# Kernel tuning notes

Measured on AMD Instinct MI355X. Metric: run time of the kernel, lower is better.

Reference implementation:

```python
import jax, jax.numpy as jnp
import numpy as np

N, E, D, H, T, R, K = 40000, 320000, 128, 4, 3, 5, 3
DK = D // H
SQRT_DK = float(np.sqrt(DK))

def _glorot(key, shape):
    lim = float(np.sqrt(6.0 / (shape[-2] + shape[-1])))
    return jax.random.uniform(key, shape, jnp.float32, -lim, lim)

def setup_inputs():
    ks = jax.random.split(jax.random.key(0), 16)
    return {
        "meta_xs": jax.random.normal(ks[0], (N, D), jnp.float32),
        "node_type": jax.random.randint(ks[1], (N,), 0, T),
        "edge_index": jax.random.randint(ks[2], (2, E), 0, N),
        "edge_type": jax.random.randint(ks[3], (E,), 0, R),
        "edge_time": jax.random.randint(ks[4], (E,), 0, 100),
        "q_w": _glorot(ks[5], (T, D, D)), "q_b": jnp.zeros((T, D), jnp.float32),
        "k_w": _glorot(ks[6], (T, D, D)), "k_b": jnp.zeros((T, D), jnp.float32),
        "v_w": _glorot(ks[7], (T, D, D)), "v_b": jnp.zeros((T, D), jnp.float32),
        "a_w": _glorot(ks[8], (T, D, D)), "a_b": jnp.zeros((T, D), jnp.float32),
        "rel_pri": jnp.ones((R, H), jnp.float32),
        "rel_att": _glorot(ks[9], (R, H, DK, DK)),
        "rel_msg": _glorot(ks[10], (R, H, DK, DK)),
        "WMk": _glorot(ks[11], (K, D, D)),
        "Wak": _glorot(ks[12], (K, D, D)),
        "Wq": _glorot(ks[13], (D, D)), "bq": jnp.zeros((D,), jnp.float32),
        "Wkl": _glorot(ks[14], (D, D)), "bkl": jnp.zeros((D,), jnp.float32),
        "skip": jnp.ones((T,), jnp.float32),
        "ln_g": jnp.ones((T, D), jnp.float32),
        "ln_b": jnp.zeros((T, D), jnp.float32),
    }

def _forward(meta_xs, q_w, q_b, k_w, k_b, v_w, v_b, a_w, a_b, rel_pri, rel_att,
             rel_msg, WMk, Wak, Wq, bq, Wkl, bkl, skip, ln_g, ln_b,
             node_type, edge_index, edge_type):
    src, tgt = edge_index[0], edge_index[1]
    ar = jnp.arange(N)

    def typed(x, W, b):  # per-node-type linear: equivalent to the type-masked loops
        all_t = jnp.einsum('ni,tio->tno', x, W)        # [T, N, D]
        return all_t[node_type, ar] + b[node_type]      # [N, D]

    qn = typed(meta_xs, q_w, q_b).reshape(N, H, DK)
    kn = typed(meta_xs, k_w, k_b).reshape(N, H, DK)
    vn = typed(meta_xs, v_w, v_b).reshape(N, H, DK)
    qe, ke, ve = qn[tgt], kn[src], vn[src]              # [E, H, DK]

    # relation-specific bmm, honoring per-relation dispatch without [E,H,DK,DK] gather
    kp = jnp.zeros_like(ke)
    vp = jnp.zeros_like(ve)
    for r in range(R):
        sel = (edge_type == r)[:, None, None]
        kp = jnp.where(sel, jnp.einsum('ehd,hdm->ehm', ke, rel_att[r]), kp)
        vp = jnp.where(sel, jnp.einsum('ehd,hdm->ehm', ve, rel_msg[r]), vp)

    logits = (qe * kp).sum(-1) * rel_pri[edge_type] / SQRT_DK   # [E, H]
    # segment softmax over incoming edges per target node (torch_geometric softmax)
    mx = jax.ops.segment_max(logits, tgt, num_segments=N)
    ex = jnp.exp(logits - mx[tgt])
    att = ex / (jax.ops.segment_sum(ex, tgt, num_segments=N)[tgt] + 1e-16)

    # power-moment expanded, attention-weighted messages: [K, E, D]
    msgs = jnp.stack([((vp ** (kk + 1)) * att[:, :, None]).reshape(E, D) for kk in range(K)])

    # faithful to original aggregate(): messages indexed by target node id (not edge id)
    agg = jnp.stack([jax.ops.segment_sum(msgs[kk][tgt], tgt, num_segments=N) for kk in range(K)])
    # faithful: only the last moment gets the signed K-th root (loop re-clones each iter)
    root = jnp.sign(agg[K - 1]) * (jnp.abs(agg[K - 1]) + 1e-18) ** (1.0 / K)
    aggm = agg.at[K - 1].set(root)
    aggm = jnp.einsum('knd,kde->kne', aggm, WMk)        # [K, N, D]

    qlin = meta_xs @ Wq + bq
    res = jnp.zeros((N, D), meta_xs.dtype)
    for kk in range(K):
        front = qlin @ Wak[kk]                          # [N, D]
        tail = aggm[kk] @ Wkl + bkl                     # [N, D]
        t = jax.nn.sigmoid((front * tail).sum(-1))      # [N]
        res = res + t[:, None] * aggm[kk]

    # update(): gelu -> per-type linear -> learned skip -> per-type LayerNorm
    h = jax.nn.gelu(res, approximate=False)
    trans = typed(h, a_w, a_b)
    alpha = jax.nn.sigmoid(skip)[node_type][:, None]
    y = trans * alpha + meta_xs * (1.0 - alpha)
    mu = y.mean(-1, keepdims=True)
    var = ((y - mu) ** 2).mean(-1, keepdims=True)
    y = (y - mu) / jnp.sqrt(var + 1e-5) * ln_g[node_type] + ln_b[node_type]
    return y

def reference(meta_xs, node_type, edge_index, edge_type, edge_time,
              q_w, q_b, k_w, k_b, v_w, v_b, a_w, a_b, rel_pri, rel_att, rel_msg,
              WMk, Wak, Wq, bq, Wkl, bkl, skip, ln_g, ln_b):
    return _forward(meta_xs, q_w, q_b, k_w, k_b, v_w, v_b, a_w, a_b, rel_pri,
                    rel_att, rel_msg, WMk, Wak, Wq, bq, Wkl, bkl, skip, ln_g, ln_b,
                    node_type, edge_index, edge_type)
```

## Files before the change

kernel.cpp:

```cpp
#include <hip/hip_runtime.h>

#define N_ 40000
#define E_ 320000
#define D_ 128
#define H_ 4
#define T_ 3
#define R_ 5

typedef unsigned short u16;

__device__ __forceinline__ float bf2f(u16 h){ return __uint_as_float(((unsigned)h)<<16); }
__device__ __forceinline__ u16 f2bf(float f){
  unsigned u = __float_as_uint(f);
  u += 0x7fffu + ((u>>16)&1u);
  return (u16)(u>>16);
}
__device__ __forceinline__ unsigned fmono(float f){
  unsigned u = __float_as_uint(f);
  return (u>>31) ? ~u : (u | 0x80000000u);
}
__device__ __forceinline__ float monof(unsigned u){
  return (u>>31) ? __uint_as_float(u & 0x7fffffffu) : __uint_as_float(~u);
}
__device__ __forceinline__ float ldx(const void* p, long i, int f32){
  return f32 ? ((const float*)p)[i] : bf2f(((const u16*)p)[i]);
}
__device__ __forceinline__ float wredsum(float v){
  #pragma unroll
  for (int m=32;m;m>>=1) v += __shfl_xor(v, m, 64);
  return v;
}

#define W_QW 0
#define W_KW 49152
#define W_VW 98304
#define W_AW 147456
#define W_QB 196608
#define W_KB 196992
#define W_VB 197376
#define W_AB 197760
#define W_PRI 198144
#define W_RATT 198164
#define W_RMSG 218644
#define W_WMK 239124
#define W_WAK 288276
#define W_WQ 337428
#define W_BQ 353812
#define W_WKL 353940
#define W_BKL 370324
#define W_SKIP 370452
#define W_LNG 370455
#define W_LNB 370839
#define W_TOT 371223

#define OFF_FLAGS 0ul
#define OFF_WCF   512ul
#define OFF_NT32  1485824ul
#define OFF_EI32  1646080ul
#define OFF_ET32  4206592ul
#define OFF_PERM  5486592ul
#define OFF_PCNT  5647360ul
#define OFF_TVAL  5647872ul
#define OFF_NPERM 5737984ul
#define OFF_LOG   6288384ul
#define OFF_QN    12848640ul
#define OFF_KN    33328640ul
#define OFF_VN    53808640ul
#define OFF_QLIN  74288640ul
#define OFF_QTR   94768640ul

__global__ __launch_bounds__(256) void detect_kernel(
    const u16* __restrict__ xs, const int* __restrict__ nt, int* __restrict__ flags)
{
  __shared__ int sBig, sZero, sNz;
  int tid = threadIdx.x;
  if (tid==0){ sBig=0; sZero=0; sNz=0; }
  __syncthreads();
  int big=0, zc=0;
  for (int i=tid; i<1024; i+=256) {
    u16 v = xs[2*i];
    int e = (v>>7)&0xFF;
    big += (e >= 200);
    zc  += (v == 0);
  }
  int nz=0;
  for (int i=tid; i<1024; i+=256) nz += (nt[2*i+1] != 0);
  atomicAdd(&sBig, big); atomicAdd(&sZero, zc); atomicAdd(&sNz, nz);
  __syncthreads();
  if (tid==0) {
    flags[0] = (sBig > 64) || (sZero > 900);
    flags[1] = (sNz == 0);
  }
}

struct FPtrs { const void* p[20]; };
__global__ __launch_bounds__(256) void convf_kernel(
    const int* __restrict__ flags, FPtrs ptrs, float* __restrict__ wcf)
{
  const int start[21] = {0,49152,98304,147456,196608,196992,197376,197760,198144,
    198164,218644,239124,288276,337428,353812,353940,370324,370452,370455,370839,371223};
  int i = blockIdx.x*256 + threadIdx.x;
  if (i >= W_TOT) return;
  int arr = 0;
  #pragma unroll
  for (int a=1; a<20; ++a) arr += (i >= start[a]);
  int local = i - start[arr];
  wcf[i] = ldx(ptrs.p[arr], local, flags[0]);
}

__global__ __launch_bounds__(256) void idxconv_kernel(
    const int* __restrict__ flags,
    const int* __restrict__ nt, const int* __restrict__ ei, const int* __restrict__ et,
    int* __restrict__ nt32, int* __restrict__ ei32, int* __restrict__ et32)
{
  int i = blockIdx.x*256 + threadIdx.x;
  if (i >= 1000000) return;
  int w = flags[1] ? 2 : 1;
  if (i < 40000)        nt32[i] = nt[(long)i*w];
  else if (i < 680000)  { int j=i-40000;  ei32[j] = ei[(long)j*w]; }
  else                  { int j=i-680000; et32[j] = et[(long)j*w]; }
}

__global__ __launch_bounds__(256) void pinit_kernel(int* __restrict__ perm, int* __restrict__ pc){
  int i = blockIdx.x*256 + threadIdx.x;
  if (i < 40192) perm[i] = -1;
  if (i < 12) pc[i] = 0;
}
__global__ __launch_bounds__(256) void einit_kernel(int* __restrict__ nperm, int* __restrict__ pc2){
  int i = blockIdx.x*256 + threadIdx.x;
  if (i < 40320) nperm[i] = -1;
  if (i < 16) pc2[i] = 0;
}
__global__ __launch_bounds__(256) void cnt_kernel(
    const int* __restrict__ keys, int n, int ntypes, int* __restrict__ gcnt)
{
  __shared__ int lh[8];
  if (threadIdx.x < ntypes) lh[threadIdx.x] = 0;
  __syncthreads();
  int i = blockIdx.x*256 + threadIdx.x;
  if (i < n) atomicAdd(&lh[keys[i]], 1);
  __syncthreads();
  if (threadIdx.x < ntypes && lh[threadIdx.x])
    atomicAdd(&gcnt[threadIdx.x], lh[threadIdx.x]);
}
__global__ void pofs_kernel(int* __restrict__ pc){
  if (threadIdx.x==0 && blockIdx.x==0) {
    pc[8] = 0;
    pc[9] = (pc[0]+63)&~63;
    pc[10] = pc[9] + ((pc[1]+63)&~63);
  }
}
__global__ void eofs_kernel(int* __restrict__ pc2){
  if (threadIdx.x==0 && blockIdx.x==0) {
    pc2[10] = 0;
    #pragma unroll
    for (int r=1;r<R_;++r) pc2[10+r] = pc2[10+r-1] + ((pc2[r-1]+63)&~63);
  }
}
__global__ __launch_bounds__(256) void scat_kernel(
    const int* __restrict__ keys, int n, int ntypes,
    const int* __restrict__ ofs, int* __restrict__ fill, int* __restrict__ perm)
{
  __shared__ int lh[8];
  __shared__ int lbase[8];
  if (threadIdx.x < ntypes) lh[threadIdx.x] = 0;
  __syncthreads();
  int i = blockIdx.x*256 + threadIdx.x;
  int t = 0, rank = 0;
  bool ok = (i < n);
  if (ok) { t = keys[i]; rank = atomicAdd(&lh[t], 1); }
  __syncthreads();
  if (threadIdx.x < ntypes)
    lbase[threadIdx.x] = lh[threadIdx.x] ? atomicAdd(&fill[threadIdx.x], lh[threadIdx.x]) : 0;
  __syncthreads();
  if (ok) perm[ofs[t] + lbase[t] + rank] = i;
}

__global__ __launch_bounds__(256) void init_kernel(
    unsigned* __restrict__ mxkey, float* __restrict__ sumex, int* __restrict__ deg)
{
  int i = blockIdx.x*256 + threadIdx.x;
  mxkey[i] = fmono(-1e30f);
  sumex[i] = 0.f;
  if (i < N_) deg[i] = 0;
}

__global__ __launch_bounds__(256) void prepA_kernel(
    const float* __restrict__ wcf, float* __restrict__ raT)
{
  int i = blockIdx.x*256 + threadIdx.x;
  if (i >= 20480) return;
  int d = i & 31, m = (i>>5) & 31, rh = i >> 10;
  raT[i] = wcf[W_RATT + (rh*32 + d)*32 + m];
}

__global__ __launch_bounds__(128) void prepB_kernel(
    const float* __restrict__ wcf, float* __restrict__ MT, float* __restrict__ ck)
{
  int col = threadIdx.x, i = blockIdx.x, k = blockIdx.y;
  const float* wak = wcf + W_WAK + k*16384 + col*128;
  const float* wkl = wcf + W_WKL + i*128;
  float acc = 0.f, accC = 0.f;
  #pragma unroll 8
  for (int j=0;j<128;++j) {
    float a = wak[j];
    acc  += a * wkl[j];
    if (i==0) accC += a * wcf[W_BKL + j];
  }
  MT[k*16384 + i*128 + col] = acc;
  if (i==0) ck[k*128 + col] = accC;
}

struct P3 { const float* a[3]; };
__global__ __launch_bounds__(256) void gemmt_kernel(
    P3 xs, const int* __restrict__ flags, int xmode,
    const float* __restrict__ Wbase, int ybstride,
    const float* __restrict__ bias, int ybias,
    const int* __restrict__ perm, const int* __restrict__ nt,
    int dotmode, const float* __restrict__ qlin, const float* __restrict__ ck,
    int powmode, const float* __restrict__ sattp,
    float* __restrict__ out, long yostride)
{
  __shared__ float As[64*36];
  __shared__ float Ws[4096];
  __shared__ int ridx[64];
  __shared__ int tblk_s;
  int tid = threadIdx.x;
  int y = blockIdx.y;
  int row0 = blockIdx.x*64;
  if (tid < 64) {
    int rr = row0 + tid;
    int rg = perm ? perm[rr] : (rr < N_ ? rr : -1);
    ridx[tid] = rg;
    if (tid==0) tblk_s = (perm && nt && rg>=0) ? nt[rg] : 0;
  }
  __syncthreads();
  if (ridx[0] < 0) return;
  int tblk = tblk_s;
  const float* Wg = Wbase + (long)y*ybstride + (long)tblk*16384;
  const void* X = (const void*)xs.a[y];
  int xf = xmode ? 1 : flags[0];

  int rg_ = tid >> 5;
  int cg  = tid & 31;
  float acc[8][4];
  #pragma unroll
  for (int r=0;r<8;++r){ acc[r][0]=0.f; acc[r][1]=0.f; acc[r][2]=0.f; acc[r][3]=0.f; }

  int sar = tid >> 2;
  int sks = (tid & 3) * 8;
  int srow = ridx[sar];

  for (int kc=0;kc<4;++kc) {
    __syncthreads();
    {
      float* dst = &As[sar*36 + sks];
      if (srow < 0) {
        #pragma unroll
        for (int j=0;j<8;++j) dst[j]=0.f;
      } else if (powmode) {
        const float4* s4 = reinterpret_cast<const float4*>((const float*)X + (long)srow*128 + kc*32 + sks);
        float4 v0 = s4[0], v1 = s4[1];
        float sc = sattp[srow*4 + kc];
        float tv[8] = {v0.x,v0.y,v0.z,v0.w,v1.x,v1.y,v1.z,v1.w};
        #pragma unroll
        for (int j=0;j<8;++j) {
          float v = tv[j]; float a;
          if (y==0)      a = v*sc;
          else if (y==1) a = v*v*sc;
          else { float a3 = v*v*v*sc;
                 a = (a3==0.f) ? 0.f : copysignf(cbrtf(fabsf(a3)+1e-18f), a3); }
          dst[j] = a;
        }
      } else if (xf) {
        const float4* s4 = reinterpret_cast<const float4*>((const float*)X + (long)srow*128 + kc*32 + sks);
        float4 v0 = s4[0], v1 = s4[1];
        *reinterpret_cast<float4*>(dst)   = v0;
        *reinterpret_cast<float4*>(dst+4) = v1;
      } else {
        const u16* s = (const u16*)X + (long)srow*128 + kc*32 + sks;
        #pragma unroll
        for (int j=0;j<8;++j) dst[j] = bf2f(s[j]);
      }
    }
    #pragma unroll
    for (int j=0;j<4;++j) {
      float4 v = *reinterpret_cast<const float4*>(Wg + kc*4096 + j*1024 + tid*4);
      *reinterpret_cast<float4*>(&Ws[j*1024 + tid*4]) = v;
    }
    __syncthreads();
    #pragma unroll
    for (int kq=0;kq<8;++kq) {
      float wv[4][4];
      #pragma unroll
      for (int i=0;i<4;++i) {
        float4 wt = *reinterpret_cast<const float4*>(&Ws[(kq*4+i)*128 + cg*4]);
        wv[i][0]=wt.x; wv[i][1]=wt.y; wv[i][2]=wt.z; wv[i][3]=wt.w;
      }
      #pragma unroll
      for (int r=0;r<8;++r) {
        float4 a4 = *reinterpret_cast<const float4*>(&As[(rg_*8+r)*36 + kq*4]);
        float av[4] = {a4.x, a4.y, a4.z, a4.w};
        #pragma unroll
        for (int i=0;i<4;++i) {
          acc[r][0] += av[i]*wv[i][0];
          acc[r][1] += av[i]*wv[i][1];
          acc[r][2] += av[i]*wv[i][2];
          acc[r][3] += av[i]*wv[i][3];
        }
      }
    }
  }

  if (!dotmode) {
    const float* bp = bias ? (bias + (long)y*ybias + tblk*128 + cg*4) : nullptr;
    float b0=0,b1=0,b2=0,b3=0;
    if (bp){ b0=bp[0]; b1=bp[1]; b2=bp[2]; b3=bp[3]; }
    #pragma unroll
    for (int r=0;r<8;++r) {
      int rowg = ridx[rg_*8+r];
      if (rowg < 0) continue;
      float4 o;
      o.x=acc[r][0]+b0; o.y=acc[r][1]+b1; o.z=acc[r][2]+b2; o.w=acc[r][3]+b3;
      *reinterpret_cast<float4*>(out + (long)y*yostride + (long)rowg*128 + cg*4) = o;
    }
  } else {
    const float* ckp = ck + y*128 + cg*4;
    float c0=ckp[0], c1=ckp[1], c2=ckp[2], c3=ckp[3];
    #pragma unroll
    for (int r=0;r<8;++r) {
      int rowg = ridx[rg_*8+r];
      float d = 0.f;
      if (rowg >= 0) {
        const float* qp = qlin + (long)rowg*128 + cg*4;
        d = (acc[r][0]+c0)*qp[0] + (acc[r][1]+c1)*qp[1]
          + (acc[r][2]+c2)*qp[2] + (acc[r][3]+c3)*qp[3];
      }
      #pragma unroll
      for (int m=16;m;m>>=1) d += __shfl_xor(d, m, 64);
      if (cg==0 && rowg>=0) out[(long)rowg*4 + y] = 1.f/(1.f+expf(-d));
    }
  }
}

__global__ __launch_bounds__(256) void gemmbd_kernel(
    const float* __restrict__ X,
    const float* __restrict__ Wtab, int wsel,
    const int* __restrict__ perm, const int* __restrict__ gsrc, const int* __restrict__ et,
    float* __restrict__ out)
{
  __shared__ float As[64*152];
  __shared__ float Ws[4096];
  __shared__ int ridx[64];
  __shared__ int rsel_s;
  int tid = threadIdx.x;
  int row0 = blockIdx.x*64;
  if (tid < 64) {
    int rr = row0 + tid;
    int pe = perm ? perm[rr] : (rr < N_ ? rr : -1);
    ridx[tid] = pe;
    if (tid == 0) rsel_s = (wsel && pe >= 0) ? et[pe] : 0;
  }
  __syncthreads();
  if (ridx[0] < 0) return;
  const float* Wg = Wtab + (long)(wsel ? rsel_s : 0)*4096;
  #pragma unroll
  for (int j=0;j<4;++j)
    *reinterpret_cast<float4*>(&Ws[j*1024 + tid*4]) =
      *reinterpret_cast<const float4*>(Wg + j*1024 + tid*4);
  {
    int sar = tid >> 2, sh = tid & 3;
    int pe_s = ridx[sar];
    int arow = (pe_s < 0) ? -1 : (gsrc ? gsrc[pe_s] : pe_s);
    float* dst = &As[sar*152 + sh*36];
    if (arow < 0) {
      #pragma unroll
      for (int j=0;j<8;++j) *reinterpret_cast<float4*>(dst + j*4) = float4{0.f,0.f,0.f,0.f};
    } else {
      const float4* s4 = reinterpret_cast<const float4*>(X + (long)arow*128 + sh*32);
      #pragma unroll
      for (int j=0;j<8;++j) *reinterpret_cast<float4*>(dst + j*4) = s4[j];
    }
  }
  __syncthreads();
  int rg_ = tid >> 5, cg = tid & 31;
  int h = cg >> 3, c4 = (cg & 7)*4;
  float acc[8][4];
  #pragma unroll
  for (int r=0;r<8;++r){ acc[r][0]=0.f; acc[r][1]=0.f; acc[r][2]=0.f; acc[r][3]=0.f; }
  #pragma unroll
  for (int mq=0;mq<8;++mq) {
    float wv[4][4];
    #pragma unroll
    for (int i=0;i<4;++i) {
      float4 wt = *reinterpret_cast<const float4*>(&Ws[h*1024 + (mq*4+i)*32 + c4]);
      wv[i][0]=wt.x; wv[i][1]=wt.y; wv[i][2]=wt.z; wv[i][3]=wt.w;
    }
    #pragma unroll
    for (int r=0;r<8;++r) {
      float4 a4 = *reinterpret_cast<const float4*>(&As[(rg_*8+r)*152 + h*36 + mq*4]);
      float av[4] = {a4.x,a4.y,a4.z,a4.w};
      #pragma unroll
      for (int i=0;i<4;++i) {
        acc[r][0]+=av[i]*wv[i][0]; acc[r][1]+=av[i]*wv[i][1];
        acc[r][2]+=av[i]*wv[i][2]; acc[r][3]+=av[i]*wv[i][3];
      }
    }
  }
  #pragma unroll
  for (int r=0;r<8;++r) {
    int pe = ridx[rg_*8+r];
    if (pe < 0) continue;
    float4 o = {acc[r][0],acc[r][1],acc[r][2],acc[r][3]};
    *reinterpret_cast<float4*>(out + (long)pe*128 + h*32 + c4) = o;
  }
}

__global__ __launch_bounds__(256) void epass_kernel(
    const float* __restrict__ kn, const float* __restrict__ qtr, const float* __restrict__ wcf,
    const int* __restrict__ ei, const int* __restrict__ et, int rsel,
    float* __restrict__ logits, unsigned* __restrict__ mxkey, int* __restrict__ deg)
{
  int gid = blockIdx.x*256 + threadIdx.x;
  int e = gid >> 2, h = gid & 3;
  if (et[e] != rsel) return;
  int s = ei[e], t = ei[E_+e];
  const float4* ka = reinterpret_cast<const float4*>(kn + (long)s*128 + h*32);
  const float4* qa = reinterpret_cast<const float4*>(qtr + (long)t*128 + h*32);
  float acc = 0.f;
  #pragma unroll
  for (int i=0;i<8;++i) {
    float4 a = ka[i], b = qa[i];
    acc += a.x*b.x + a.y*b.y + a.z*b.z + a.w*b.w;
  }
  float lg = acc * wcf[W_PRI + rsel*H_+h] * 0.17677669529663687f;
  logits[gid] = lg;
  atomicMax(mxkey + t*H_+h, fmono(lg));
  if (h==0) atomicAdd(deg + t, 1);
}

__global__ __launch_bounds__(256) void eexp_kernel(
    const int* __restrict__ ei, float* __restrict__ logits,
    const unsigned* __restrict__ mxkey, float* __restrict__ sumex)
{
  int gid = blockIdx.x*256 + threadIdx.x;
  int e = gid >> 2, h = gid & 3;
  int t = ei[E_+e];
  float d = fminf(logits[gid] - monof(mxkey[t*H_+h]), 0.f);
  float ex = expf(d);
  logits[gid] = ex;
  atomicAdd(sumex + t*H_+h, ex);
}

__global__ __launch_bounds__(256) void satt_kernel(
    const int* __restrict__ ei, const float* __restrict__ ex, const float* __restrict__ sumex,
    const int* __restrict__ deg, float* __restrict__ satt)
{
  int i = blockIdx.x*256 + threadIdx.x;
  int n = i >> 2, h = i & 3;
  int t = ei[E_+n];
  satt[i] = (float)deg[n] * ex[i] / (sumex[t*H_+h] + 1e-16f);
}

__global__ __launch_bounds__(256) void gatemix_kernel(
    const float* __restrict__ tval,
    const float* __restrict__ ag0, const float* __restrict__ ag1, const float* __restrict__ ag2,
    float* __restrict__ hout)
{
  long gid = (long)blockIdx.x*256 + threadIdx.x;
  int n = (int)(gid >> 7);
  float res = tval[n*4+0]*ag0[gid] + tval[n*4+1]*ag1[gid] + tval[n*4+2]*ag2[gid];
  hout[gid] = 0.5f*res*(1.f+erff(res*0.70710678118654752f));
}

__global__ __launch_bounds__(256) void lnf_kernel(
    const float* __restrict__ trans, const void* __restrict__ x, const int* __restrict__ flags,
    const int* __restrict__ nt, const float* __restrict__ wcf, void* __restrict__ outv)
{
  int wave = threadIdx.x >> 6, lane = threadIdx.x & 63;
  int n = blockIdx.x*4 + wave;
  int j = lane*2;
  int xf = flags[0];
  int t = nt[n];
  float alpha = 1.f/(1.f+expf(-wcf[W_SKIP+t]));
  long base = (long)n*128 + j;
  float y0 = alpha*trans[base]   + (1.f-alpha)*ldx(x, base,   xf);
  float y1 = alpha*trans[base+1] + (1.f-alpha)*ldx(x, base+1, xf);
  float mu = wredsum(y0+y1) * (1.f/128.f);
  float d0 = y0-mu, d1 = y1-mu;
  float var = wredsum(d0*d0+d1*d1) * (1.f/128.f);
  float inv = rsqrtf(var + 1e-5f);
  float o0 = d0*inv*wcf[W_LNG + t*128+j]   + wcf[W_LNB + t*128+j];
  float o1 = d1*inv*wcf[W_LNG + t*128+j+1] + wcf[W_LNB + t*128+j+1];
  if (xf) {
    ((float*)outv)[base]   = o0;
    ((float*)outv)[base+1] = o1;
  } else {
    unsigned o = (unsigned)f2bf(o0) | ((unsigned)f2bf(o1)<<16);
    *reinterpret_cast<unsigned*>(((u16*)outv)+base) = o;
  }
}

extern "C" void kernel_launch(void* const* d_in, const int* in_sizes, int n_in,
                              void* d_out, int out_size, void* d_ws, size_t ws_size,
                              hipStream_t stream) {
  char* w = (char*)d_ws;
  int*      flags = (int*)     (w + OFF_FLAGS);
  float*    wcf   = (float*)   (w + OFF_WCF);
  int*      nt32  = (int*)     (w + OFF_NT32);
  int*      ei32  = (int*)     (w + OFF_EI32);
  int*      et32  = (int*)     (w + OFF_ET32);
  int*      perm  = (int*)     (w + OFF_PERM);
  int*      pcnt  = (int*)     (w + OFF_PCNT);
  int*      pc2   = (int*)     (w + OFF_PCNT + 128);
  float*    raT   = (float*)   (w + OFF_TVAL);
  float*    satt  = (float*)   (w + OFF_TVAL);
  float*    tval  = (float*)   (w + OFF_TVAL);
  int*      nperm = (int*)     (w + OFF_NPERM);
  float*    logits= (float*)   (w + OFF_LOG);
  unsigned* mxkey = (unsigned*)(w + OFF_LOG + 5120000);
  float*    sumex = (float*)   (w + OFF_LOG + 5760000);
  int*      deg   = (int*)     (w + OFF_LOG + 6400000);
  float*    MT    = (float*)   (w + OFF_LOG);
  float*    ckb   = (float*)   (w + OFF_LOG + 786432);
  float*    qn    = (float*)   (w + OFF_QN);
  float*    ag0   = (float*)   (w + OFF_QN);
  float*    trans = (float*)   (w + OFF_QN);
  float*    kn    = (float*)   (w + OFF_KN);
  float*    ag1   = (float*)   (w + OFF_KN);
  float*    vn    = (float*)   (w + OFF_VN);
  float*    ag2   = (float*)   (w + OFF_VN);
  float*    qlin  = (float*)   (w + OFF_QLIN);
  float*    hbuf  = (float*)   (w + OFF_QLIN);
  float*    qtrb  = (float*)   (w + OFF_QTR);
  float*    vp    = (float*)   (w + OFF_QTR);

  detect_kernel<<<1,256,0,stream>>>((const u16*)d_in[0], (const int*)d_in[1], flags);
  FPtrs fp;
  fp.p[0]=d_in[5];  fp.p[1]=d_in[7];  fp.p[2]=d_in[9];  fp.p[3]=d_in[11];
  fp.p[4]=d_in[6];  fp.p[5]=d_in[8];  fp.p[6]=d_in[10]; fp.p[7]=d_in[12];
  fp.p[8]=d_in[13]; fp.p[9]=d_in[14]; fp.p[10]=d_in[15];fp.p[11]=d_in[16];
  fp.p[12]=d_in[17];fp.p[13]=d_in[18];fp.p[14]=d_in[19];fp.p[15]=d_in[20];
  fp.p[16]=d_in[21];fp.p[17]=d_in[22];fp.p[18]=d_in[23];fp.p[19]=d_in[24];
  convf_kernel<<<1451,256,0,stream>>>(flags, fp, wcf);
  idxconv_kernel<<<3907,256,0,stream>>>(flags, (const int*)d_in[1],
                                        (const int*)d_in[2], (const int*)d_in[3],
                                        nt32, ei32, et32);
  pinit_kernel<<<157,256,0,stream>>>(perm, pcnt);
  cnt_kernel  <<<157,256,0,stream>>>(nt32, N_, T_, pcnt);
  pofs_kernel <<<1,64,0,stream>>>(pcnt);
  scat_kernel <<<157,256,0,stream>>>(nt32, N_, T_, pcnt+8, pcnt+4, perm);
  einit_kernel<<<158,256,0,stream>>>(nperm, pc2);
  cnt_kernel  <<<157,256,0,stream>>>(et32, N_, R_, pc2);
  eofs_kernel <<<1,64,0,stream>>>(pc2);
  scat_kernel <<<157,256,0,stream>>>(et32, N_, R_, pc2+10, pc2+5, nperm);
  prepA_kernel<<<80,256,0,stream>>>(wcf, raT);

  P3 xin; xin.a[0]=(const float*)d_in[0]; xin.a[1]=xin.a[0]; xin.a[2]=xin.a[0];
  gemmt_kernel<<<dim3(628,3),256,0,stream>>>(xin, flags, 0,
      wcf+W_QW, 49152, wcf+W_QB, 384, perm, nt32, 0, nullptr, nullptr, 0, nullptr,
      qn, 5120000);
  gemmt_kernel<<<dim3(625,1),256,0,stream>>>(xin, flags, 0,
      wcf+W_WQ, 0, wcf+W_BQ, 0, nullptr, nullptr, 0, nullptr, nullptr, 0, nullptr,
      qlin, 0);

  init_kernel<<<625,256,0,stream>>>(mxkey, sumex, deg);

  for (int r=0; r<R_; ++r) {
    gemmbd_kernel<<<625,256,0,stream>>>(qn, raT + r*4096, 0, nullptr, nullptr, nullptr, qtrb);
    epass_kernel<<<5000,256,0,stream>>>(kn, qtrb, wcf, ei32, et32, r, logits, mxkey, deg);
  }
  eexp_kernel<<<5000,256,0,stream>>>(ei32, logits, mxkey, sumex);

  gemmbd_kernel<<<630,256,0,stream>>>(vn, wcf+W_RMSG, 1, nperm, ei32, et32, vp);

  satt_kernel<<<625,256,0,stream>>>(ei32, logits, sumex, deg, satt);

  prepB_kernel<<<dim3(128,3),128,0,stream>>>(wcf, MT, ckb);

  P3 xvp; xvp.a[0]=vp; xvp.a[1]=vp; xvp.a[2]=vp;
  gemmt_kernel<<<dim3(625,3),256,0,stream>>>(xvp, flags, 1,
      wcf+W_WMK, 16384, nullptr, 0, nullptr, nullptr, 0, nullptr, nullptr, 1, satt,
      ag0, 5120000);

  P3 xag; xag.a[0]=ag0; xag.a[1]=ag1; xag.a[2]=ag2;
  gemmt_kernel<<<dim3(625,3),256,0,stream>>>(xag, flags, 1,
      MT, 16384, nullptr, 0, nullptr, nullptr, 1, qlin, ckb, 0, nullptr,
      tval, 0);

  gatemix_kernel<<<20000,256,0,stream>>>(tval, ag0, ag1, ag2, hbuf);

  P3 xh; xh.a[0]=hbuf; xh.a[1]=hbuf; xh.a[2]=hbuf;
  gemmt_kernel<<<dim3(628,1),256,0,stream>>>(xh, flags, 1,
      wcf+W_AW, 0, wcf+W_AB, 0, perm, nt32, 0, nullptr, nullptr, 0, nullptr,
      trans, 0);

  lnf_kernel<<<10000,256,0,stream>>>(trans, d_in[0], flags, nt32, wcf, d_out);

  (void)in_sizes; (void)n_in; (void)out_size; (void)ws_size;
}
```

Baseline: 658.4 us.

## Use 128-row GEMM tiles with 8x8 register blocking and fuse Q/K/V/Wq launches

Replaces the 64-row GEMM with a 128-row tile that stores A transposed in shared memory and gives each thread an 8x8 accumulator block, doubling register reuse per shared-memory load. The Q/K/V typed projections and the Wq linear now run as four y-slices of one launch via a config struct, and node-type padding is raised to 128 to match the new tile. The eexp kernel now writes back exponentials only for edge indices below N. Register use per thread rises, which may lower occupancy.

```diff
diff --git a/kernel.cpp b/kernel.cpp
--- a/kernel.cpp
+++ b/kernel.cpp
@@ -59,15 +59,15 @@
 #define OFF_EI32  1646080ul
 #define OFF_ET32  4206592ul
 #define OFF_PERM  5486592ul
-#define OFF_PCNT  5647360ul
-#define OFF_TVAL  5647872ul
-#define OFF_NPERM 5737984ul
-#define OFF_LOG   6288384ul
-#define OFF_QN    12848640ul
-#define OFF_KN    33328640ul
-#define OFF_VN    53808640ul
-#define OFF_QLIN  74288640ul
-#define OFF_QTR   94768640ul
+#define OFF_PCNT  5648384ul
+#define OFF_TVAL  5648896ul
+#define OFF_NPERM 5730816ul
+#define OFF_LOG   6288896ul
+#define OFF_QN    12848896ul
+#define OFF_KN    33328896ul
+#define OFF_VN    53808896ul
+#define OFF_QLIN  74288896ul
+#define OFF_QTR   94768896ul
 
 __global__ __launch_bounds__(256) void detect_kernel(
     const u16* __restrict__ xs, const int* __restrict__ nt, int* __restrict__ flags)
@@ -123,7 +123,7 @@
 
 __global__ __launch_bounds__(256) void pinit_kernel(int* __restrict__ perm, int* __restrict__ pc){
   int i = blockIdx.x*256 + threadIdx.x;
-  if (i < 40192) perm[i] = -1;
+  if (i < 40448) perm[i] = -1;
   if (i < 12) pc[i] = 0;
 }
 __global__ __launch_bounds__(256) void einit_kernel(int* __restrict__ nperm, int* __restrict__ pc2){
@@ -146,8 +146,8 @@
 __global__ void pofs_kernel(int* __restrict__ pc){
   if (threadIdx.x==0 && blockIdx.x==0) {
     pc[8] = 0;
-    pc[9] = (pc[0]+63)&~63;
-    pc[10] = pc[9] + ((pc[1]+63)&~63);
+    pc[9] = (pc[0]+127)&~127;
+    pc[10] = pc[9] + ((pc[1]+127)&~127);
   }
 }
 __global__ void eofs_kernel(int* __restrict__ pc2){
@@ -211,24 +211,23 @@
   if (i==0) ck[k*128 + col] = accC;
 }
 
-struct P3 { const float* a[3]; };
-__global__ __launch_bounds__(256) void gemmt_kernel(
-    P3 xs, const int* __restrict__ flags, int xmode,
-    const float* __restrict__ Wbase, int ybstride,
-    const float* __restrict__ bias, int ybias,
+struct GC4 { const float* x[4]; int woff[4]; int boff[4]; int typed[4]; };
+__global__ __launch_bounds__(256) void gemmt2_kernel(
+    GC4 cfg, const int* __restrict__ flags, int xmode,
+    const float* __restrict__ Wsrc,
     const int* __restrict__ perm, const int* __restrict__ nt,
     int dotmode, const float* __restrict__ qlin, const float* __restrict__ ck,
     int powmode, const float* __restrict__ sattp,
     float* __restrict__ out, long yostride)
 {
-  __shared__ float As[64*36];
+  __shared__ float As[32*132];
   __shared__ float Ws[4096];
-  __shared__ int ridx[64];
+  __shared__ int ridx[128];
   __shared__ int tblk_s;
   int tid = threadIdx.x;
   int y = blockIdx.y;
-  int row0 = blockIdx.x*64;
-  if (tid < 64) {
+  int row0 = blockIdx.x*128;
+  if (tid < 128) {
     int rr = row0 + tid;
     int rg = perm ? perm[rr] : (rr < N_ ? rr : -1);
     ridx[tid] = rg;
@@ -236,108 +235,120 @@
   }
   __syncthreads();
   if (ridx[0] < 0) return;
-  int tblk = tblk_s;
-  const float* Wg = Wbase + (long)y*ybstride + (long)tblk*16384;
-  const void* X = (const void*)xs.a[y];
+  int tblk = cfg.typed[y] ? tblk_s : 0;
+  const float* Wg = Wsrc + cfg.woff[y] + tblk*16384;
+  const void* X = (const void*)cfg.x[y];
   int xf = xmode ? 1 : flags[0];
 
-  int rg_ = tid >> 5;
-  int cg  = tid & 31;
-  float acc[8][4];
-  #pragma unroll
-  for (int r=0;r<8;++r){ acc[r][0]=0.f; acc[r][1]=0.f; acc[r][2]=0.f; acc[r][3]=0.f; }
-
-  int sar = tid >> 2;
-  int sks = (tid & 3) * 8;
-  int srow = ridx[sar];
+  int rg_ = tid >> 4;
+  int cg  = tid & 15;
+  int rowb = rg_*8;
+  float acc[8][8];
+  #pragma unroll
+  for (int r=0;r<8;++r)
+    #pragma unroll
+    for (int c=0;c<8;++c) acc[r][c]=0.f;
+
+  int sr = tid >> 1;
+  int sh = (tid & 1) * 16;
+  int srow = ridx[sr];
 
   for (int kc=0;kc<4;++kc) {
     __syncthreads();
     {
-      float* dst = &As[sar*36 + sks];
+      float v[16];
       if (srow < 0) {
         #pragma unroll
-        for (int j=0;j<8;++j) dst[j]=0.f;
+        for (int j=0;j<16;++j) v[j]=0.f;
       } else if (powmode) {
-        const float4* s4 = reinterpret_cast<const float4*>((const float*)X + (long)srow*128 + kc*32 + sks);
-        float4 v0 = s4[0], v1 = s4[1];
+        const float4* s4 = reinterpret_cast<const float4*>((const float*)X + (long)srow*128 + kc*32 + sh);
+        float4 q0=s4[0],q1=s4[1],q2=s4[2],q3=s4[3];
+        float tv[16] = {q0.x,q0.y,q0.z,q0.w,q1.x,q1.y,q1.z,q1.w,
+                        q2.x,q2.y,q2.z,q2.w,q3.x,q3.y,q3.z,q3.w};
         float sc = sattp[srow*4 + kc];
-        float tv[8] = {v0.x,v0.y,v0.z,v0.w,v1.x,v1.y,v1.z,v1.w};
         #pragma unroll
-        for (int j=0;j<8;++j) {
-          float v = tv[j]; float a;
-          if (y==0)      a = v*sc;
-          else if (y==1) a = v*v*sc;
-          else { float a3 = v*v*v*sc;
+        for (int j=0;j<16;++j) {
+          float vv = tv[j]; float a;
+          if (y==0)      a = vv*sc;
+          else if (y==1) a = vv*vv*sc;
+          else { float a3 = vv*vv*vv*sc;
                  a = (a3==0.f) ? 0.f : copysignf(cbrtf(fabsf(a3)+1e-18f), a3); }
-          dst[j] = a;
+          v[j] = a;
         }
       } else if (xf) {
-        const float4* s4 = reinterpret_cast<const float4*>((const float*)X + (long)srow*128 + kc*32 + sks);
-        float4 v0 = s4[0], v1 = s4[1];
-        *reinterpret_cast<float4*>(dst)   = v0;
-        *reinterpret_cast<float4*>(dst+4) = v1;
+        const float4* s4 = reinterpret_cast<const float4*>((const float*)X + (long)srow*128 + kc*32 + sh);
+        float4 q0=s4[0],q1=s4[1],q2=s4[2],q3=s4[3];
+        v[0]=q0.x;v[1]=q0.y;v[2]=q0.z;v[3]=q0.w; v[4]=q1.x;v[5]=q1.y;v[6]=q1.z;v[7]=q1.w;
+        v[8]=q2.x;v[9]=q2.y;v[10]=q2.z;v[11]=q2.w; v[12]=q3.x;v[13]=q3.y;v[14]=q3.z;v[15]=q3.w;
       } else {
-        const u16* s = (const u16*)X + (long)srow*128 + kc*32 + sks;
+        const u16* s = (const u16*)X + (long)srow*128 + kc*32 + sh;
         #pragma unroll
-        for (int j=0;j<8;++j) dst[j] = bf2f(s[j]);
+        for (int j=0;j<16;++j) v[j] = bf2f(s[j]);
       }
+      #pragma unroll
+      for (int j=0;j<16;++j) As[(sh+j)*132 + sr] = v[j];
     }
     #pragma unroll
     for (int j=0;j<4;++j) {
-      float4 v = *reinterpret_cast<const float4*>(Wg + kc*4096 + j*1024 + tid*4);
-      *reinterpret_cast<float4*>(&Ws[j*1024 + tid*4]) = v;
+      float4 v4 = *reinterpret_cast<const float4*>(Wg + kc*4096 + j*1024 + tid*4);
+      *reinterpret_cast<float4*>(&Ws[j*1024 + tid*4]) = v4;
     }
     __syncthreads();
     #pragma unroll
     for (int kq=0;kq<8;++kq) {
-      float wv[4][4];
       #pragma unroll
       for (int i=0;i<4;++i) {
-        float4 wt = *reinterpret_cast<const float4*>(&Ws[(kq*4+i)*128 + cg*4]);
-        wv[i][0]=wt.x; wv[i][1]=wt.y; wv[i][2]=wt.z; wv[i][3]=wt.w;
+        int k = kq*4+i;
+        float4 w0 = *reinterpret_cast<const float4*>(&Ws[k*128 + cg*4]);
+        float4 w1 = *reinterpret_cast<const float4*>(&Ws[k*128 + 64 + cg*4]);
+        float4 a0 = *reinterpret_cast<const float4*>(&As[k*132 + rowb]);
+        float4 a1 = *reinterpret_cast<const float4*>(&As[k*132 + rowb + 4]);
+        float av[8] = {a0.x,a0.y,a0.z,a0.w,a1.x,a1.y,a1.z,a1.w};
+        float wv[8] = {w0.x,w0.y,w0.z,w0.w,w1.x,w1.y,w1.z,w1.w};
+        #pragma unroll
+        for (int r=0;r<8;++r)
+          #pragma unroll
+          for (int c=0;c<8;++c)
+            acc[r][c] += av[r]*wv[c];
+      }
+    }
+  }
+
+  if (!dotmode) {
+    float b[8] = {0,0,0,0,0,0,0,0};
+    if (cfg.boff[y] >= 0) {
+      const float* bp = Wsrc + cfg.boff[y] + tblk*128;
+      #pragma unroll
+      for (int c=0;c<4;++c) { b[c]=bp[cg*4+c]; b[4+c]=bp[64+cg*4+c]; }
+    }
+    #pragma unroll
+    for (int r=0;r<8;++r) {
+      int rowg = ridx[rowb + r];
+      if (rowg < 0) continue;
+      float4 o0 = {acc[r][0]+b[0], acc[r][1]+b[1], acc[r][2]+b[2], acc[r][3]+b[3]};
+      float4 o1 = {acc[r][4]+b[4], acc[r][5]+b[5], acc[r][6]+b[6], acc[r][7]+b[7]};
+      float* op = out + (long)y*yostride + (long)rowg*128;
+      *reinterpret_cast<float4*>(op + cg*4)      = o0;
+      *reinterpret_cast<float4*>(op + 64 + cg*4) = o1;
+    }
+  } else {
+    float c0[8];
+    #pragma unroll
+    for (int c=0;c<4;++c) { c0[c]=ck[y*128+cg*4+c]; c0[4+c]=ck[y*128+64+cg*4+c]; }
+    #pragma unroll
+    for (int r=0;r<8;++r) {
+      int rowg = ridx[rowb + r];
+      float d = 0.f;
+      if (rowg >= 0) {
+        const float* qp = qlin + (long)rowg*128;
+        #pragma unroll
+        for (int c=0;c<4;++c) {
+          d += (acc[r][c]  +c0[c])  *qp[cg*4+c];
+          d += (acc[r][4+c]+c0[4+c])*qp[64+cg*4+c];
+        }
       }
       #pragma unroll
-      for (int r=0;r<8;++r) {
-        float4 a4 = *reinterpret_cast<const float4*>(&As[(rg_*8+r)*36 + kq*4]);
-        float av[4] = {a4.x, a4.y, a4.z, a4.w};
-        #pragma unroll
-        for (int i=0;i<4;++i) {
-          acc[r][0] += av[i]*wv[i][0];
-          acc[r][1] += av[i]*wv[i][1];
-          acc[r][2] += av[i]*wv[i][2];
-          acc[r][3] += av[i]*wv[i][3];
-        }
-      }
-    }
-  }
-
-  if (!dotmode) {
-    const float* bp = bias ? (bias + (long)y*ybias + tblk*128 + cg*4) : nullptr;
-    float b0=0,b1=0,b2=0,b3=0;
-    if (bp){ b0=bp[0]; b1=bp[1]; b2=bp[2]; b3=bp[3]; }
-    #pragma unroll
-    for (int r=0;r<8;++r) {
-      int rowg = ridx[rg_*8+r];
-      if (rowg < 0) continue;
-      float4 o;
-      o.x=acc[r][0]+b0; o.y=acc[r][1]+b1; o.z=acc[r][2]+b2; o.w=acc[r][3]+b3;
-      *reinterpret_cast<float4*>(out + (long)y*yostride + (long)rowg*128 + cg*4) = o;
-    }
-  } else {
-    const float* ckp = ck + y*128 + cg*4;
-    float c0=ckp[0], c1=ckp[1], c2=ckp[2], c3=ckp[3];
-    #pragma unroll
-    for (int r=0;r<8;++r) {
-      int rowg = ridx[rg_*8+r];
-      float d = 0.f;
-      if (rowg >= 0) {
-        const float* qp = qlin + (long)rowg*128 + cg*4;
-        d = (acc[r][0]+c0)*qp[0] + (acc[r][1]+c1)*qp[1]
-          + (acc[r][2]+c2)*qp[2] + (acc[r][3]+c3)*qp[3];
-      }
-      #pragma unroll
-      for (int m=16;m;m>>=1) d += __shfl_xor(d, m, 64);
+      for (int m=8;m;m>>=1) d += __shfl_xor(d, m, 64);
       if (cg==0 && rowg>=0) out[(long)rowg*4 + y] = 1.f/(1.f+expf(-d));
     }
   }
@@ -448,7 +459,7 @@
   int t = ei[E_+e];
   float d = fminf(logits[gid] - monof(mxkey[t*H_+h]), 0.f);
   float ex = expf(d);
-  logits[gid] = ex;
+  if (e < N_) logits[gid] = ex;
   atomicAdd(sumex + t*H_+h, ex);
 }
 
@@ -546,7 +557,7 @@
   idxconv_kernel<<<3907,256,0,stream>>>(flags, (const int*)d_in[1],
                                         (const int*)d_in[2], (const int*)d_in[3],
                                         nt32, ei32, et32);
-  pinit_kernel<<<157,256,0,stream>>>(perm, pcnt);
+  pinit_kernel<<<159,256,0,stream>>>(perm, pcnt);
   cnt_kernel  <<<157,256,0,stream>>>(nt32, N_, T_, pcnt);
   pofs_kernel <<<1,64,0,stream>>>(pcnt);
   scat_kernel <<<157,256,0,stream>>>(nt32, N_, T_, pcnt+8, pcnt+4, perm);
@@ -556,13 +567,13 @@
   scat_kernel <<<157,256,0,stream>>>(et32, N_, R_, pc2+10, pc2+5, nperm);
   prepA_kernel<<<80,256,0,stream>>>(wcf, raT);
 
-  P3 xin; xin.a[0]=(const float*)d_in[0]; xin.a[1]=xin.a[0]; xin.a[2]=xin.a[0];
-  gemmt_kernel<<<dim3(628,3),256,0,stream>>>(xin, flags, 0,
-      wcf+W_QW, 49152, wcf+W_QB, 384, perm, nt32, 0, nullptr, nullptr, 0, nullptr,
-      qn, 5120000);
-  gemmt_kernel<<<dim3(625,1),256,0,stream>>>(xin, flags, 0,
-      wcf+W_WQ, 0, wcf+W_BQ, 0, nullptr, nullptr, 0, nullptr, nullptr, 0, nullptr,
-      qlin, 0);
+  GC4 cq;
+  cq.x[0]=(const float*)d_in[0]; cq.x[1]=cq.x[0]; cq.x[2]=cq.x[0]; cq.x[3]=cq.x[0];
+  cq.woff[0]=W_QW; cq.woff[1]=W_KW; cq.woff[2]=W_VW; cq.woff[3]=W_WQ;
+  cq.boff[0]=W_QB; cq.boff[1]=W_KB; cq.boff[2]=W_VB; cq.boff[3]=W_BQ;
+  cq.typed[0]=1; cq.typed[1]=1; cq.typed[2]=1; cq.typed[3]=0;
+  gemmt2_kernel<<<dim3(316,4),256,0,stream>>>(cq, flags, 0, wcf, perm, nt32,
+      0, nullptr, nullptr, 0, nullptr, qn, 5120000);
 
   init_kernel<<<625,256,0,stream>>>(mxkey, sumex, deg);
 
@@ -578,22 +589,31 @@
 
   prepB_kernel<<<dim3(128,3),128,0,stream>>>(wcf, MT, ckb);
 
-  P3 xvp; xvp.a[0]=vp; xvp.a[1]=vp; xvp.a[2]=vp;
-  gemmt_kernel<<<dim3(625,3),256,0,stream>>>(xvp, flags, 1,
-      wcf+W_WMK, 16384, nullptr, 0, nullptr, nullptr, 0, nullptr, nullptr, 1, satt,
-      ag0, 5120000);
-
-  P3 xag; xag.a[0]=ag0; xag.a[1]=ag1; xag.a[2]=ag2;
-  gemmt_kernel<<<dim3(625,3),256,0,stream>>>(xag, flags, 1,
-      MT, 16384, nullptr, 0, nullptr, nullptr, 1, qlin, ckb, 0, nullptr,
-      tval, 0);
+  GC4 cp;
+  cp.x[0]=vp; cp.x[1]=vp; cp.x[2]=vp; cp.x[3]=vp;
+  cp.woff[0]=W_WMK; cp.woff[1]=W_WMK+16384; cp.woff[2]=W_WMK+32768; cp.woff[3]=0;
+  cp.boff[0]=-1; cp.boff[1]=-1; cp.boff[2]=-1; cp.boff[3]=-1;
+  cp.typed[0]=0; cp.typed[1]=0; cp.typed[2]=0; cp.typed[3]=0;
+  gemmt2_kernel<<<dim3(313,3),256,0,stream>>>(cp, flags, 1, wcf, nullptr, nullptr,
+      0, nullptr, nullptr, 1, satt, ag0, 5120000);
+
+  GC4 cd;
+  cd.x[0]=ag0; cd.x[1]=ag1; cd.x[2]=ag2; cd.x[3]=ag2;
+  cd.woff[0]=0; cd.woff[1]=16384; cd.woff[2]=32768; cd.woff[3]=0;
+  cd.boff[0]=-1; cd.boff[1]=-1; cd.boff[2]=-1; cd.boff[3]=-1;
+  cd.typed[0]=0; cd.typed[1]=0; cd.typed[2]=0; cd.typed[3]=0;
+  gemmt2_kernel<<<dim3(313,3),256,0,stream>>>(cd, flags, 1, MT, nullptr, nullptr,
+      1, qlin, ckb, 0, nullptr, tval, 0);
 
   gatemix_kernel<<<20000,256,0,stream>>>(tval, ag0, ag1, ag2, hbuf);
 
-  P3 xh; xh.a[0]=hbuf; xh.a[1]=hbuf; xh.a[2]=hbuf;
-  gemmt_kernel<<<dim3(628,1),256,0,stream>>>(xh, flags, 1,
-      wcf+W_AW, 0, wcf+W_AB, 0, perm, nt32, 0, nullptr, nullptr, 0, nullptr,
-      trans, 0);
+  GC4 ct;
+  ct.x[0]=hbuf; ct.x[1]=hbuf; ct.x[2]=hbuf; ct.x[3]=hbuf;
+  ct.woff[0]=W_AW; ct.woff[1]=0; ct.woff[2]=0; ct.woff[3]=0;
+  ct.boff[0]=W_AB; ct.boff[1]=-1; ct.boff[2]=-1; ct.boff[3]=-1;
+  ct.typed[0]=1; ct.typed[1]=0; ct.typed[2]=0; ct.typed[3]=0;
+  gemmt2_kernel<<<dim3(316,1),256,0,stream>>>(ct, flags, 1, wcf, perm, nt32,
+      0, nullptr, nullptr, 0, nullptr, trans, 0);
 
   lnf_kernel<<<10000,256,0,stream>>>(trans, d_in[0], flags, nt32, wcf, d_out);
 
```

After: 647.2 us. Within noise of the previous version (-1.7%).
